# Optimization experiments

Measured on AMD Instinct MI355X. Metric: run time of the kernel, lower is better.

## Reference

```python
import jax, jax.numpy as jnp
import numpy as np

B, H, W, C = 32, 256, 256, 3
FLAT = (H // 4) * (W // 4) * 64  # 64*64*64 = 262144 after two stride-2 SAME convs


def _conv(x, k, b, stride):
    y = jax.lax.conv_general_dilated(
        x, k, (stride, stride), 'SAME',
        dimension_numbers=('NHWC', 'HWIO', 'NHWC'))
    return jax.nn.relu(y + b)


def _grid_sample(img, theta):
    # STN: build normalized affine grid from theta [B,2,3], bilinear sample with
    # zero padding for out-of-bounds (GridSampler2D semantics).
    b, h, w, c = img.shape
    xs = (2.0 * jnp.arange(w, dtype=img.dtype) + 1.0) / w - 1.0
    ys = (2.0 * jnp.arange(h, dtype=img.dtype) + 1.0) / h - 1.0
    X, Y = jnp.meshgrid(xs, ys)                      # [H,W]
    base = jnp.stack([X, Y, jnp.ones_like(X)], -1)   # [H,W,3]
    g = jnp.einsum('bij,hwj->bhwi', theta, base)     # [B,H,W,2] (x,y) in [-1,1]
    px = (g[..., 0] + 1.0) * 0.5 * w - 0.5
    py = (g[..., 1] + 1.0) * 0.5 * h - 0.5
    x0 = jnp.floor(px); y0 = jnp.floor(py)
    wx1 = px - x0; wx0 = 1.0 - wx1
    wy1 = py - y0; wy0 = 1.0 - wy1

    bidx = jnp.arange(b)[:, None, None]

    def gather(yi, xi):
        valid = (xi >= 0) & (xi < w) & (yi >= 0) & (yi < h)
        xc = jnp.clip(xi, 0, w - 1).astype(jnp.int32)
        yc = jnp.clip(yi, 0, h - 1).astype(jnp.int32)
        v = img[bidx, yc, xc]                        # [B,H,W,C]
        return v * valid[..., None].astype(img.dtype)

    out = (gather(y0, x0) * (wy0 * wx0)[..., None]
           + gather(y0, x0 + 1) * (wy0 * wx1)[..., None]
           + gather(y0 + 1, x0) * (wy1 * wx0)[..., None]
           + gather(y0 + 1, x0 + 1) * (wy1 * wx1)[..., None])
    return out


def setup_inputs() -> dict:
    key = jax.random.key(0)
    ks = jax.random.split(key, 9)
    s = 0.05
    return {
        'inputs': jax.random.uniform(ks[0], (B, H, W, C), jnp.float32),
        'k1': jax.random.normal(ks[1], (3, 3, C, 32), jnp.float32) * s,
        'b1': jnp.zeros((32,), jnp.float32),
        'k2': jax.random.normal(ks[2], (3, 3, 32, 64), jnp.float32) * s,
        'b2': jnp.zeros((64,), jnp.float32),
        'w1': jax.random.normal(ks[3], (FLAT, 128), jnp.float32) * 0.002,
        'd1': jnp.zeros((128,), jnp.float32),
        'w2': jax.random.normal(ks[4], (128, 6), jnp.float32) * s,
        'd2': jnp.asarray([1, 0, 0, 0, 1, 0], jnp.float32),  # identity-ish bias
    }


def reference(inputs, k1, b1, k2, b2, w1, d1, w2, d2):
    x = _conv(inputs, k1, b1, 2)          # [B,H/2,W/2,32]
    x = _conv(x, k2, b2, 2)               # [B,H/4,W/4,64]
    x = x.reshape(x.shape[0], -1)         # [B,FLAT]
    x = jax.nn.relu(x @ w1 + d1)          # [B,128]
    theta = (x @ w2 + d2).reshape(-1, 2, 3)
    return _grid_sample(inputs, theta)
```

## Files before the change

### kernel.cpp

```cpp
#include <hip/hip_runtime.h>

#define IN_H 256
#define IN_W 256
#define C0   3
#define C1   32
#define H1   128
#define C2   64
#define H2   64
#define NB   32
#define K_FLAT (H2*H2*C2)
#define NHID 128

__global__ __launch_bounds__(128)
void conv1_k(const float* __restrict__ in, const float* __restrict__ k1,
             const float* __restrict__ b1, float* __restrict__ a1) {
  const int ox = threadIdx.x;
  const int oy = blockIdx.x;
  const int b  = blockIdx.y;
  float acc[C1];
#pragma unroll
  for (int co = 0; co < C1; ++co) acc[co] = b1[co];

  for (int dy = 0; dy < 3; ++dy) {
    const int iy  = 2*oy + dy;
    const bool rok = iy < IN_H;
    const int iyc = rok ? iy : (IN_H-1);
    for (int dx = 0; dx < 3; ++dx) {
      const int ix  = 2*ox + dx;
      const bool ok = rok && (ix < IN_W);
      const int ixc = (ix < IN_W) ? ix : (IN_W-1);
      const float* ip = in + ((size_t)(b*IN_H + iyc)*IN_W + ixc)*C0;
      const float v0 = ok ? ip[0] : 0.f;
      const float v1 = ok ? ip[1] : 0.f;
      const float v2 = ok ? ip[2] : 0.f;
      const float* wp = k1 + (size_t)((dy*3+dx)*C0)*C1;
#pragma unroll
      for (int co = 0; co < C1; ++co)
        acc[co] = fmaf(v0, wp[co],
                  fmaf(v1, wp[C1+co],
                  fmaf(v2, wp[2*C1+co], acc[co])));
    }
  }
  float* op = a1 + ((size_t)(b*H1 + oy)*H1 + ox)*C1;
#pragma unroll
  for (int g = 0; g < 8; ++g) {
    float4 o;
    o.x = fmaxf(acc[4*g+0], 0.f);
    o.y = fmaxf(acc[4*g+1], 0.f);
    o.z = fmaxf(acc[4*g+2], 0.f);
    o.w = fmaxf(acc[4*g+3], 0.f);
    ((float4*)op)[g] = o;
  }
}

__global__ __launch_bounds__(256)
void conv2_k(const float* __restrict__ a1, const float* __restrict__ k2,
             const float* __restrict__ b2, float* __restrict__ a2) {
  const int tid = threadIdx.x;
  const int ox  = tid & 63;
  const int cg16 = __builtin_amdgcn_readfirstlane((tid >> 6) * 16);
  const int oy  = blockIdx.x;
  const int b   = blockIdx.y;

  float acc[16];
#pragma unroll
  for (int co = 0; co < 16; ++co) acc[co] = b2[cg16 + co];

  for (int dy = 0; dy < 3; ++dy) {
    const int iy  = 2*oy + dy;
    const bool rok = iy < H1;
    const int iyc = rok ? iy : (H1-1);
    for (int dx = 0; dx < 3; ++dx) {
      const int ix  = 2*ox + dx;
      const bool ok = rok && (ix < H1);
      const int ixc = (ix < H1) ? ix : (H1-1);
      const float4* ip = (const float4*)(a1 + ((size_t)(b*H1 + iyc)*H1 + ixc)*C1);
      const float* wp = k2 + (size_t)((dy*3+dx)*C1)*C2 + cg16;
#pragma unroll
      for (int g = 0; g < 8; ++g) {
        float4 t = ip[g];
        if (!ok) t = make_float4(0.f,0.f,0.f,0.f);
#pragma unroll
        for (int cc = 0; cc < 4; ++cc) {
          const float vv = (cc==0) ? t.x : (cc==1) ? t.y : (cc==2) ? t.z : t.w;
          const float* wr = wp + (size_t)(g*4+cc)*C2;
#pragma unroll
          for (int co = 0; co < 16; ++co) acc[co] = fmaf(vv, wr[co], acc[co]);
        }
      }
    }
  }
  float* op = a2 + ((size_t)(b*H2 + oy)*H2 + ox)*C2 + cg16;
#pragma unroll
  for (int g = 0; g < 4; ++g) {
    float4 o;
    o.x = fmaxf(acc[4*g+0], 0.f);
    o.y = fmaxf(acc[4*g+1], 0.f);
    o.z = fmaxf(acc[4*g+2], 0.f);
    o.w = fmaxf(acc[4*g+3], 0.f);
    ((float4*)op)[g] = o;
  }
}

#define FC1_G   1024
#define KSPAN   (K_FLAT / FC1_G)

__global__ __launch_bounds__(256)
void fc1_partial_k(const float* __restrict__ a2, const float* __restrict__ w1,
                   float* __restrict__ partial) {
  __shared__ __align__(16) float xT[KSPAN*36];
  const int tid = threadIdx.x;
  const int q   = tid & 31;
  const int bo  = tid >> 5;
  const int k0  = blockIdx.x * KSPAN;

  {
    const int lb  = tid >> 3;
    const int lkq = tid & 7;
#pragma unroll
    for (int j = 0; j < 8; ++j) {
      const int k4 = lkq*4 + j*32;
      float4 t = *(const float4*)(a2 + (size_t)lb*K_FLAT + k0 + k4);
      xT[(k4+0)*36 + lb] = t.x;
      xT[(k4+1)*36 + lb] = t.y;
      xT[(k4+2)*36 + lb] = t.z;
      xT[(k4+3)*36 + lb] = t.w;
    }
  }
  __syncthreads();

  float4 a0 = make_float4(0.f,0.f,0.f,0.f), a1v = a0, a2v = a0, a3v = a0;
#pragma unroll 4
  for (int k = 0; k < KSPAN; ++k) {
    const float4 w4 = *(const float4*)(w1 + (size_t)(k0 + k)*NHID + 4*q);
    const float4 xb = *(const float4*)&xT[k*36 + 4*bo];
    a0.x = fmaf(xb.x, w4.x, a0.x); a0.y = fmaf(xb.x, w4.y, a0.y);
    a0.z = fmaf(xb.x, w4.z, a0.z); a0.w = fmaf(xb.x, w4.w, a0.w);
    a1v.x = fmaf(xb.y, w4.x, a1v.x); a1v.y = fmaf(xb.y, w4.y, a1v.y);
    a1v.z = fmaf(xb.y, w4.z, a1v.z); a1v.w = fmaf(xb.y, w4.w, a1v.w);
    a2v.x = fmaf(xb.z, w4.x, a2v.x); a2v.y = fmaf(xb.z, w4.y, a2v.y);
    a2v.z = fmaf(xb.z, w4.z, a2v.z); a2v.w = fmaf(xb.z, w4.w, a2v.w);
    a3v.x = fmaf(xb.w, w4.x, a3v.x); a3v.y = fmaf(xb.w, w4.y, a3v.y);
    a3v.z = fmaf(xb.w, w4.z, a3v.z); a3v.w = fmaf(xb.w, w4.w, a3v.w);
  }

  float* pp = partial + (size_t)blockIdx.x*(NB*NHID) + 4*q;
  *(float4*)(pp + (4*bo+0)*NHID) = a0;
  *(float4*)(pp + (4*bo+1)*NHID) = a1v;
  *(float4*)(pp + (4*bo+2)*NHID) = a2v;
  *(float4*)(pp + (4*bo+3)*NHID) = a3v;
}

__global__ __launch_bounds__(128)
void fc1_reduce1_k(const float* __restrict__ partial, float* __restrict__ partial2) {
  const int t  = blockIdx.x*128 + threadIdx.x;
  const int gc = blockIdx.y;
  float s = 0.f;
#pragma unroll 8
  for (int g = gc*128; g < gc*128+128; ++g) s += partial[(size_t)g*(NB*NHID) + t];
  partial2[(size_t)gc*(NB*NHID) + t] = s;
}

__global__ __launch_bounds__(256)
void fc1_reduce2_k(const float* __restrict__ partial2, const float* __restrict__ d1,
                   float* __restrict__ h) {
  const int t = blockIdx.x*256 + threadIdx.x;
  float s = 0.f;
#pragma unroll
  for (int gc = 0; gc < 8; ++gc) s += partial2[(size_t)gc*(NB*NHID) + t];
  h[t] = fmaxf(s + d1[t & (NHID-1)], 0.f);
}

__global__ __launch_bounds__(192)
void theta_k(const float* __restrict__ h, const float* __restrict__ w2,
             const float* __restrict__ d2, float* __restrict__ theta) {
  const int t = threadIdx.x;
  if (t >= NB*6) return;
  const int b = t / 6, j = t % 6;
  float s = d2[j];
  for (int n = 0; n < NHID; ++n) s = fmaf(h[b*NHID + n], w2[n*6 + j], s);
  theta[t] = s;
}

__global__ __launch_bounds__(256)
void sample_k(const float* __restrict__ img, const float* __restrict__ theta,
              float* __restrict__ out) {
  const int x = threadIdx.x;
  const int y = blockIdx.x & (IN_H-1);
  const int b = blockIdx.x >> 8;
  const float* tp = theta + b*6;
  const float t0 = tp[0], t1 = tp[1], t2 = tp[2];
  const float t3 = tp[3], t4 = tp[4], t5 = tp[5];

  const float xs = (2.f*x + 1.f)*(1.f/IN_W) - 1.f;
  const float ys = (2.f*y + 1.f)*(1.f/IN_H) - 1.f;
  const float gx = fmaf(t0, xs, fmaf(t1, ys, t2));
  const float gy = fmaf(t3, xs, fmaf(t4, ys, t5));
  const float px = fmaf(gx + 1.f, 0.5f*IN_W, -0.5f);
  const float py = fmaf(gy + 1.f, 0.5f*IN_H, -0.5f);

  const float x0f = floorf(px), y0f = floorf(py);
  const int ix0 = (int)x0f, iy0 = (int)y0f;
  const float wx1 = px - x0f, wx0 = 1.f - wx1;
  const float wy1 = py - y0f, wy0 = 1.f - wy1;

  float r = 0.f, g = 0.f, bl = 0.f;
  const float* ib = img + (size_t)b*IN_H*IN_W*C0;

  auto tap = [&](int yi, int xi, float w) {
    const bool v = (xi >= 0) && (xi < IN_W) && (yi >= 0) && (yi < IN_H);
    const int xc = xi < 0 ? 0 : (xi > IN_W-1 ? IN_W-1 : xi);
    const int yc = yi < 0 ? 0 : (yi > IN_H-1 ? IN_H-1 : yi);
    const float* p = ib + ((size_t)yc*IN_W + xc)*C0;
    if (v) {
      r  = fmaf(w, p[0], r);
      g  = fmaf(w, p[1], g);
      bl = fmaf(w, p[2], bl);
    }
  };
  tap(iy0,   ix0,   wy0*wx0);
  tap(iy0,   ix0+1, wy0*wx1);
  tap(iy0+1, ix0,   wy1*wx0);
  tap(iy0+1, ix0+1, wy1*wx1);

  float* op = out + ((size_t)(b*IN_H + y)*IN_W + x)*C0;
  op[0] = r; op[1] = g; op[2] = bl;
}

extern "C" void kernel_launch(void* const* d_in, const int* in_sizes, int n_in,
                              void* d_out, int out_size, void* d_ws, size_t ws_size,
                              hipStream_t stream) {
  const float* in = (const float*)d_in[0];
  const float* k1 = (const float*)d_in[1];
  const float* b1 = (const float*)d_in[2];
  const float* k2 = (const float*)d_in[3];
  const float* b2 = (const float*)d_in[4];
  const float* w1 = (const float*)d_in[5];
  const float* d1 = (const float*)d_in[6];
  const float* w2 = (const float*)d_in[7];
  const float* d2 = (const float*)d_in[8];
  float* out = (float*)d_out;
  float* ws  = (float*)d_ws;

  float* a1      = ws;
  float* a2      = ws + (size_t)16777216;
  float* partial = ws;
  float* part2   = ws + (size_t)4194304;
  float* h       = ws + (size_t)4227072;
  float* th      = ws + (size_t)4231168;

  hipLaunchKernelGGL(conv1_k,       dim3(128, 32), dim3(128), 0, stream, in, k1, b1, a1);
  hipLaunchKernelGGL(conv2_k,       dim3(64, 32),  dim3(256), 0, stream, a1, k2, b2, a2);
  hipLaunchKernelGGL(fc1_partial_k, dim3(FC1_G),   dim3(256), 0, stream, a2, w1, partial);
  hipLaunchKernelGGL(fc1_reduce1_k, dim3(32, 8),   dim3(128), 0, stream, partial, part2);
  hipLaunchKernelGGL(fc1_reduce2_k, dim3(16),      dim3(256), 0, stream, part2, d1, h);
  hipLaunchKernelGGL(theta_k,       dim3(1),       dim3(192), 0, stream, h, w2, d2, th);
  hipLaunchKernelGGL(sample_k,      dim3(NB*IN_H), dim3(256), 0, stream, in, th, out);
}
```

Baseline: 404.1 us.

## Store conv1 output in parity-split channel-planar layout for coalesced conv2 reads

conv1 now writes its activations in a [b][y][x-parity][channel][x/2] layout, and each thread computes 16 of the 32 output channels, which doubles the threads per block. conv2 then reads one scalar per input channel with consecutive lanes touching consecutive addresses, instead of strided float4 loads across 128-byte pixel records. The conv loops are also fully unrolled, and the theta dot product is split into four independent accumulators. In exchange, conv1 now loads each input pixel twice (once per channel-half thread) and makes 16 scalar stores where it previously made float4 stores.

```diff
diff --git a/kernel.cpp b/kernel.cpp
--- a/kernel.cpp
+++ b/kernel.cpp
@@ -11,20 +11,27 @@
 #define K_FLAT (H2*H2*C2)
 #define NHID 128
 
-__global__ __launch_bounds__(128)
+#define A1_IDX(b,y,p,ci,x2) (((((size_t)(b)*H1 + (y))*2 + (p))*C1 + (ci))*64 + (x2))
+
+__global__ __launch_bounds__(256)
 void conv1_k(const float* __restrict__ in, const float* __restrict__ k1,
-             const float* __restrict__ b1, float* __restrict__ a1) {
-  const int ox = threadIdx.x;
-  const int oy = blockIdx.x;
-  const int b  = blockIdx.y;
-  float acc[C1];
-#pragma unroll
-  for (int co = 0; co < C1; ++co) acc[co] = b1[co];
-
+             const float* __restrict__ b1, float* __restrict__ a1p) {
+  const int tid = threadIdx.x;
+  const int ox  = tid & 127;
+  const int cg  = __builtin_amdgcn_readfirstlane((tid >> 7) * 16);
+  const int oy  = blockIdx.x;
+  const int b   = blockIdx.y;
+
+  float acc[16];
+#pragma unroll
+  for (int co = 0; co < 16; ++co) acc[co] = b1[cg + co];
+
+#pragma unroll
   for (int dy = 0; dy < 3; ++dy) {
     const int iy  = 2*oy + dy;
     const bool rok = iy < IN_H;
     const int iyc = rok ? iy : (IN_H-1);
+#pragma unroll
     for (int dx = 0; dx < 3; ++dx) {
       const int ix  = 2*ox + dx;
       const bool ok = rok && (ix < IN_W);
@@ -33,28 +40,23 @@
       const float v0 = ok ? ip[0] : 0.f;
       const float v1 = ok ? ip[1] : 0.f;
       const float v2 = ok ? ip[2] : 0.f;
-      const float* wp = k1 + (size_t)((dy*3+dx)*C0)*C1;
-#pragma unroll
-      for (int co = 0; co < C1; ++co)
+      const float* wp = k1 + (size_t)((dy*3+dx)*C0)*C1 + cg;
+#pragma unroll
+      for (int co = 0; co < 16; ++co)
         acc[co] = fmaf(v0, wp[co],
                   fmaf(v1, wp[C1+co],
                   fmaf(v2, wp[2*C1+co], acc[co])));
     }
   }
-  float* op = a1 + ((size_t)(b*H1 + oy)*H1 + ox)*C1;
-#pragma unroll
-  for (int g = 0; g < 8; ++g) {
-    float4 o;
-    o.x = fmaxf(acc[4*g+0], 0.f);
-    o.y = fmaxf(acc[4*g+1], 0.f);
-    o.z = fmaxf(acc[4*g+2], 0.f);
-    o.w = fmaxf(acc[4*g+3], 0.f);
-    ((float4*)op)[g] = o;
-  }
-}
-
-__global__ __launch_bounds__(256)
-void conv2_k(const float* __restrict__ a1, const float* __restrict__ k2,
+  const int p  = ox & 1;
+  const int x2 = ox >> 1;
+#pragma unroll
+  for (int co = 0; co < 16; ++co)
+    a1p[A1_IDX(b, oy, p, cg + co, x2)] = fmaxf(acc[co], 0.f);
+}
+
+__global__ __launch_bounds__(256)
+void conv2_k(const float* __restrict__ a1p, const float* __restrict__ k2,
              const float* __restrict__ b2, float* __restrict__ a2) {
   const int tid = threadIdx.x;
   const int ox  = tid & 63;
@@ -66,27 +68,26 @@
 #pragma unroll
   for (int co = 0; co < 16; ++co) acc[co] = b2[cg16 + co];
 
+#pragma unroll
   for (int dy = 0; dy < 3; ++dy) {
     const int iy  = 2*oy + dy;
     const bool rok = iy < H1;
     const int iyc = rok ? iy : (H1-1);
+#pragma unroll
     for (int dx = 0; dx < 3; ++dx) {
-      const int ix  = 2*ox + dx;
-      const bool ok = rok && (ix < H1);
-      const int ixc = (ix < H1) ? ix : (H1-1);
-      const float4* ip = (const float4*)(a1 + ((size_t)(b*H1 + iyc)*H1 + ixc)*C1);
+      const int p   = dx & 1;
+      const int x2  = ox + (dx >> 1);
+      const bool ok = rok && (x2 < 64);
+      const int x2c = (x2 < 64) ? x2 : 63;
+      const float* ip = a1p + A1_IDX(b, iyc, p, 0, x2c);
       const float* wp = k2 + (size_t)((dy*3+dx)*C1)*C2 + cg16;
 #pragma unroll
-      for (int g = 0; g < 8; ++g) {
-        float4 t = ip[g];
-        if (!ok) t = make_float4(0.f,0.f,0.f,0.f);
-#pragma unroll
-        for (int cc = 0; cc < 4; ++cc) {
-          const float vv = (cc==0) ? t.x : (cc==1) ? t.y : (cc==2) ? t.z : t.w;
-          const float* wr = wp + (size_t)(g*4+cc)*C2;
-#pragma unroll
-          for (int co = 0; co < 16; ++co) acc[co] = fmaf(vv, wr[co], acc[co]);
-        }
+      for (int ci = 0; ci < C1; ++ci) {
+        float v = ip[(size_t)ci*64];
+        v = ok ? v : 0.f;
+        const float* wr = wp + (size_t)ci*C2;
+#pragma unroll
+        for (int co = 0; co < 16; ++co) acc[co] = fmaf(v, wr[co], acc[co]);
       }
     }
   }
@@ -177,9 +178,14 @@
   const int t = threadIdx.x;
   if (t >= NB*6) return;
   const int b = t / 6, j = t % 6;
-  float s = d2[j];
-  for (int n = 0; n < NHID; ++n) s = fmaf(h[b*NHID + n], w2[n*6 + j], s);
-  theta[t] = s;
+  float s0 = 0.f, s1 = 0.f, s2 = 0.f, s3 = 0.f;
+  for (int n = 0; n < NHID; n += 4) {
+    s0 = fmaf(h[b*NHID + n+0], w2[(n+0)*6 + j], s0);
+    s1 = fmaf(h[b*NHID + n+1], w2[(n+1)*6 + j], s1);
+    s2 = fmaf(h[b*NHID + n+2], w2[(n+2)*6 + j], s2);
+    s3 = fmaf(h[b*NHID + n+3], w2[(n+3)*6 + j], s3);
+  }
+  theta[t] = (s0 + s1) + (s2 + s3) + d2[j];
 }
 
 __global__ __launch_bounds__(256)
@@ -242,15 +248,15 @@
   float* out = (float*)d_out;
   float* ws  = (float*)d_ws;
 
-  float* a1      = ws;
+  float* a1p     = ws;
   float* a2      = ws + (size_t)16777216;
   float* partial = ws;
   float* part2   = ws + (size_t)4194304;
   float* h       = ws + (size_t)4227072;
   float* th      = ws + (size_t)4231168;
 
-  hipLaunchKernelGGL(conv1_k,       dim3(128, 32), dim3(128), 0, stream, in, k1, b1, a1);
-  hipLaunchKernelGGL(conv2_k,       dim3(64, 32),  dim3(256), 0, stream, a1, k2, b2, a2);
+  hipLaunchKernelGGL(conv1_k,       dim3(128, 32), dim3(256), 0, stream, in, k1, b1, a1p);
+  hipLaunchKernelGGL(conv2_k,       dim3(64, 32),  dim3(256), 0, stream, a1p, k2, b2, a2);
   hipLaunchKernelGGL(fc1_partial_k, dim3(FC1_G),   dim3(256), 0, stream, a2, w1, partial);
   hipLaunchKernelGGL(fc1_reduce1_k, dim3(32, 8),   dim3(128), 0, stream, partial, part2);
   hipLaunchKernelGGL(fc1_reduce2_k, dim3(16),      dim3(256), 0, stream, part2, d1, h);
```

Result: slower. 424.6 us (+5.1%).
